# Kernel optimization log

Measured on AMD Instinct MI355X. Metric: run time of the kernel, lower is better.

The kernel has to match this reference:

```python
import jax, jax.numpy as jnp
import numpy as np

B, S, H = 2, 1024, 2048
D = 256          # index_dimension = min(index.embedding_dimension, hidden_size)
R = 32           # LoRA rank
K = 4            # index_k neighbors per query token
N_DB = 100000    # rows in the external index


def setup_inputs() -> dict:
    key = jax.random.key(0)
    ks = jax.random.split(key, 7)
    return {
        "hidden_states": jax.random.normal(ks[0], (B, S, H), jnp.float32),
        "db_keys": jax.random.normal(ks[1], (N_DB, D), jnp.float32),
        "db_values": jax.random.normal(ks[2], (N_DB, D), jnp.float32),
        "wq_in": jax.random.normal(ks[3], (H, R), jnp.float32) * 0.02,
        "wq_out": jax.random.normal(ks[4], (R, D), jnp.float32) * 0.02,
        "wv_in": jax.random.normal(ks[5], (D, R), jnp.float32) * 0.02,
        "wv_out": jax.random.normal(ks[6], (R, H), jnp.float32) * 0.02,
    }


def reference(hidden_states, db_keys, db_values, wq_in, wq_out, wv_in, wv_out):
    b, s, h = hidden_states.shape
    d = wq_out.shape[1]
    # query LoRA projection: hidden -> r -> index_dim
    q = (hidden_states @ wq_in) @ wq_out            # [B, S, D]

    # external k-NN lookup (exact L2 top-k over index table), no_grad in torch
    qf = q.reshape(b * s, d)                        # [B*S, D]
    qn = jnp.sum(qf * qf, axis=-1, keepdims=True)   # [B*S, 1]
    kn = jnp.sum(db_keys * db_keys, axis=-1)        # [N_DB]
    dist = qn - 2.0 * (qf @ db_keys.T) + kn[None, :]  # [B*S, N_DB]
    _, idx = jax.lax.top_k(-dist, K)                # [B*S, K] nearest neighbors

    # gather KV and reshape to [B, S*K, D] (matches torch view calls)
    kv_key = jax.lax.stop_gradient(db_keys[idx]).reshape(b, s * K, d)
    kv_val = jax.lax.stop_gradient(db_values[idx]).reshape(b, s * K, d)

    # SDPA, is_causal=True with Lq != Lk: top-left aligned tril mask (j <= i)
    scale = 1.0 / np.sqrt(d).astype(np.float32)
    scores = jnp.einsum('bqd,bkd->bqk', q, kv_key) * scale  # [B, S, S*K]
    mask = jnp.arange(s * K)[None, :] <= jnp.arange(s)[:, None]
    scores = jnp.where(mask[None, :, :], scores, jnp.finfo(scores.dtype).min)
    attn = jax.nn.softmax(scores, axis=-1)
    out = jnp.einsum('bqk,bkd->bqd', attn, kv_val)  # [B, S, D]

    # value LoRA projection: index_dim -> r -> hidden
    return (out @ wv_in) @ wv_out                   # [B, S, H]
```

## Files before the change

### kernel.cpp

```cpp
#include <hip/hip_runtime.h>
#include <cfloat>

#define B_   2
#define S_   1024
#define H_   2048
#define D_   256
#define R_   32
#define K_   4
#define NDB_ 100000

#define TSEL 256
#define NSEL (B_ * TSEL)

#define NCHUNK     112
#define CHUNK_ROWS 896
#define TILES      7
#define NT         128
#define MTM        32
#define QB_N       (NSEL / MTM)
#define MT         64
#define KC         64
#define LSTR       68

#define NEG_INF  (-3.0e38f)
#define IDX_MAX  0x7fffffff

#define TQ 4

#define OFF_Q     0
#define OFF_KN    0x200000
#define OFF_PS    0x280000
#define OFF_PI    0x360000
#define OFF_KVT   0x480000
#define OFF_KVV   0x680000
#define OFF_IDX   0x880000
#define OFF_DBK16 0xA00000

typedef unsigned short ushort_t;
typedef unsigned int   uint_t;
typedef __attribute__((ext_vector_type(8)))  __bf16 bf16x8;
typedef __attribute__((ext_vector_type(16))) float  f32x16;

__device__ __forceinline__ void ins4(float sc, int n, float s[4], int id[4]) {
  if (sc > s[3] || (sc == s[3] && n < id[3])) {
    s[3] = sc; id[3] = n;
#pragma unroll
    for (int k = 3; k > 0; --k) {
      if (s[k] > s[k - 1] || (s[k] == s[k - 1] && id[k] < id[k - 1])) {
        float ts = s[k]; s[k] = s[k - 1]; s[k - 1] = ts;
        int ti = id[k]; id[k] = id[k - 1]; id[k - 1] = ti;
      }
    }
  }
}

__device__ __forceinline__ uint_t bfpack(float a, float b) {
  uint_t ua = __float_as_uint(a), ub = __float_as_uint(b);
  ua = (ua + 0x7fffu + ((ua >> 16) & 1u)) >> 16;
  ub = (ub + 0x7fffu + ((ub >> 16) & 1u)) >> 16;
  return ua | (ub << 16);
}

__global__ __launch_bounds__(256) void k_prep(
    const float* __restrict__ hidden, const float* __restrict__ wq_in,
    const float* __restrict__ wq_out, float* __restrict__ q,
    const float* __restrict__ dbk, float* __restrict__ kn,
    ushort_t* __restrict__ dbk16T) {
  __shared__ __align__(16) char sm[32768];
  const int t = threadIdx.x;
  if (blockIdx.x < B_ * S_) {
    float* hrow = (float*)sm;
    float (*part)[R_] = (float(*)[R_])(sm + 8192);
    float* q1 = (float*)(sm + 9216);
    const int m = blockIdx.x;
    const float* hp = hidden + (size_t)m * H_;
    ((float4*)hrow)[t]       = ((const float4*)hp)[t];
    ((float4*)hrow)[t + 256] = ((const float4*)hp)[t + 256];
    __syncthreads();
    const int r = t & 31, c = t >> 5;
    float p = 0.f;
#pragma unroll 4
    for (int e = c * 256; e < c * 256 + 256; ++e)
      p = fmaf(hrow[e], wq_in[(size_t)e * R_ + r], p);
    part[c][r] = p;
    __syncthreads();
    if (t < R_) {
      float s = 0.f;
#pragma unroll
      for (int cc = 0; cc < 8; ++cc) s += part[cc][t];
      q1[t] = s;
    }
    __syncthreads();
    float acc = 0.f;
#pragma unroll
    for (int rr = 0; rr < R_; ++rr) acc = fmaf(q1[rr], wq_out[rr * D_ + t], acc);
    q[(size_t)m * D_ + t] = acc;
  } else {
    float* sT = (float*)sm;
    const int n32 = blockIdx.x - B_ * S_;
    {
      const int r = t >> 3, tc = t & 7;
      const float* rp = dbk + (size_t)(n32 * 32 + r) * D_;
      float s = 0.f;
#pragma unroll
      for (int k = 0; k < 8; ++k) {
        const int sl = tc + 8 * k;
        const float4 v = ((const float4*)rp)[sl];
        *(float4*)&sT[(r * 64 + (sl ^ (r & 7))) * 4] = v;
        s += v.x * v.x + v.y * v.y + v.z * v.z + v.w * v.w;
      }
      s += __shfl_down(s, 4, 8);
      s += __shfl_down(s, 2, 8);
      s += __shfl_down(s, 1, 8);
      if (tc == 0) kn[n32 * 32 + r] = s;
    }
    __syncthreads();
    {
      const int l = t & 63, w = t >> 6;
      const int row = l & 31, hc = l >> 5;
      uint4* dst = (uint4*)dbk16T + (size_t)n32 * 1024;
#pragma unroll
      for (int kk = 0; kk < 4; ++kk) {
        const int ks = kk * 4 + w;
        const int c = 2 * ks + hc;
        const int s0 = (2 * c) ^ (row & 7), s1 = (2 * c + 1) ^ (row & 7);
        const float4 a = *(const float4*)&sT[(row * 64 + s0) * 4];
        const float4 b = *(const float4*)&sT[(row * 64 + s1) * 4];
        uint4 pk;
        pk.x = bfpack(a.x, a.y); pk.y = bfpack(a.z, a.w);
        pk.z = bfpack(b.x, b.y); pk.w = bfpack(b.z, b.w);
        dst[(size_t)ks * 64 + l] = pk;
      }
    }
  }
}

__global__ __launch_bounds__(256) void k_compute_q(
    const float* __restrict__ hidden, const float* __restrict__ wq_in,
    const float* __restrict__ wq_out, float* __restrict__ q) {
  __shared__ float hrow[H_];
  __shared__ float part[8][R_];
  __shared__ float q1[R_];
  const int m = blockIdx.x;
  const int t = threadIdx.x;
  const float* hp = hidden + (size_t)m * H_;
  ((float4*)hrow)[t]       = ((const float4*)hp)[t];
  ((float4*)hrow)[t + 256] = ((const float4*)hp)[t + 256];
  __syncthreads();
  const int r = t & 31, c = t >> 5;
  float p = 0.f;
#pragma unroll 4
  for (int e = c * 256; e < c * 256 + 256; ++e)
    p = fmaf(hrow[e], wq_in[(size_t)e * R_ + r], p);
  part[c][r] = p;
  __syncthreads();
  if (t < R_) {
    float s = 0.f;
#pragma unroll
    for (int cc = 0; cc < 8; ++cc) s += part[cc][t];
    q1[t] = s;
  }
  __syncthreads();
  float acc = 0.f;
#pragma unroll
  for (int rr = 0; rr < R_; ++rr) acc = fmaf(q1[rr], wq_out[rr * D_ + t], acc);
  q[(size_t)m * D_ + t] = acc;
}

__global__ __launch_bounds__(256) void k_kn(const float* __restrict__ dbk,
                                            float* __restrict__ kn) {
  const int w = threadIdx.x >> 6, l = threadIdx.x & 63;
  const int n = blockIdx.x * 4 + w;
  if (n >= NDB_) return;
  const float4 v = ((const float4*)(dbk + (size_t)n * D_))[l];
  float s = v.x * v.x + v.y * v.y + v.z * v.z + v.w * v.w;
#pragma unroll
  for (int off = 32; off; off >>= 1) s += __shfl_down(s, off);
  if (l == 0) kn[n] = s;
}

__global__ __launch_bounds__(256, 7) void k_knn_mfma(
    const float* __restrict__ q, const ushort_t* __restrict__ dbk16T,
    const float* __restrict__ kn, float* __restrict__ pscore,
    int* __restrict__ pidx) {
  __shared__ __align__(16) char smem[16384 + CHUNK_ROWS * 4];
  ushort_t* sA  = (ushort_t*)smem;
  float*    knL = (float*)(smem + 16384);

  const int fid = blockIdx.x;
  const int xcd = fid & 7, idx8 = fid >> 3;
  const int chunk = xcd + 8 * (idx8 % 14);
  const int qb = idx8 / 14;

  const int tid = threadIdx.x;
  const int wv = tid >> 6, ln = tid & 63;
  const int lm = ln & 31, lh = ln >> 5;
  const int row_base = chunk * CHUNK_ROWS;

  {
    const int m = tid & 31, cg = tid >> 5;
    const int sq = qb * MTM + m;
    const float* qp = q + ((size_t)((sq >> 8) * S_ + (sq & 255))) * D_;
#pragma unroll
    for (int cc = 0; cc < 4; ++cc) {
      const int c = cg * 4 + cc;
      const float4 v0 = *(const float4*)(qp + c * 8);
      const float4 v1 = *(const float4*)(qp + c * 8 + 4);
      uint4 pk;
      pk.x = bfpack(v0.x, v0.y); pk.y = bfpack(v0.z, v0.w);
      pk.z = bfpack(v1.x, v1.y); pk.w = bfpack(v1.z, v1.w);
      *(uint4*)&sA[(m * 32 + (c ^ (m & 7))) * 8] = pk;
    }
  }
  for (int j = tid; j < CHUNK_ROWS; j += 256) {
    int rr = row_base + j; if (rr >= NDB_) rr = NDB_ - 1;
    knL[j] = kn[rr];
  }
  __syncthreads();

  float s40[4]; int i40[4];
#pragma unroll
  for (int k = 0; k < 4; ++k) { s40[k] = NEG_INF; i40[k] = IDX_MAX; }

  const int sw = lm & 7;
  const int abase0 = lm * 32;
  const int nbase = wv * 32 + 4 * lh;

  for (int tile = 0; tile < TILES; ++tile) {
    const int row0 = row_base + tile * NT;
    if (row0 >= NDB_) break;
    const int nw = row0 + wv * 32;
    if (nw >= NDB_) continue;

    f32x16 acc0;
#pragma unroll
    for (int r = 0; r < 16; ++r) acc0[r] = 0.f;

    const ushort_t* gw = dbk16T + (size_t)(nw >> 5) * 8192 + (size_t)ln * 8;
#pragma unroll
    for (int ks = 0; ks < 16; ++ks) {
      const bf16x8 bb = *(const bf16x8*)(gw + ks * 512);
      const int cs = (2 * ks + lh) ^ sw;
      const bf16x8 a0 = *(const bf16x8*)&sA[(abase0 + cs) * 8];
      acc0 = __builtin_amdgcn_mfma_f32_32x32x16_bf16(bb, a0, acc0, 0, 0, 0);
    }

#pragma unroll
    for (int g = 0; g < 4; ++g) {
      float v0[4]; int nn[4];
#pragma unroll
      for (int j = 0; j < 4; ++j) {
        const int r = g * 4 + j;
        const int off = (r & 3) + 8 * (r >> 2);
        const int nloc = nbase + off;
        const float knv = knL[tile * 128 + nloc];
        const int n = row0 + nloc;
        nn[j] = n;
        const float x0 = fmaf(2.f, acc0[r], -knv);
        v0[j] = (n < NDB_) ? x0 : NEG_INF;
      }
      const float m0 = fmaxf(fmaxf(v0[0], v0[1]), fmaxf(v0[2], v0[3]));
      if (m0 >= s40[3]) {
#pragma unroll
        for (int j = 0; j < 4; ++j) ins4(v0[j], nn[j], s40, i40);
      }
    }
  }

  __syncthreads();
  float* cs = (float*)smem;
  int*   ci = (int*)(smem + 4096);
  {
    const int st = wv * 2 + lh;
#pragma unroll
    for (int k = 0; k < 4; ++k) {
      cs[(lm * 8 + st) * 4 + k] = s40[k];
      ci[(lm * 8 + st) * 4 + k] = i40[k];
    }
  }
  __syncthreads();
  if (tid < MTM) {
    float fs[4]; int fi[4];
#pragma unroll
    for (int k = 0; k < 4; ++k) { fs[k] = NEG_INF; fi[k] = IDX_MAX; }
    for (int c = 0; c < 32; ++c)
      ins4(cs[tid * 32 + c], ci[tid * 32 + c], fs, fi);
    const int sq = qb * MTM + tid;
    float* po = pscore + ((size_t)sq * NCHUNK + chunk) * 4;
    int*   io = pidx   + ((size_t)sq * NCHUNK + chunk) * 4;
#pragma unroll
    for (int k = 0; k < 4; ++k) { po[k] = fs[k]; io[k] = fi[k]; }
  }
}

__global__ __launch_bounds__(256) void k_knn_partial(
    const float* __restrict__ q, const float* __restrict__ dbk,
    const float* __restrict__ kn, float* __restrict__ pscore,
    int* __restrict__ pidx) {
  __shared__ float smem[3 * KC * LSTR];
  float* sA  = smem;
  float* sB0 = smem + KC * LSTR;
  float* sB1 = smem + 2 * KC * LSTR;
  const int tid = threadIdx.x;
  const int tx = tid & 15, ty = tid >> 4;
  const int chunk = blockIdx.x, qb = blockIdx.y;
  const int arq = tid >> 2;
  const int aqd = (tid & 3) * 4;
  const int brk = tid >> 1;
  const int bh  = tid & 1;
  const int bcol = ((brk >> 3) << 2) | (brk & 3);
  float* sBw = (brk & 4) ? sB1 : sB0;
  const int sq_a = qb * MT + arq;
  const float* qsrc = q + ((size_t)((sq_a >> 8) * S_ + (sq_a & 255))) * D_;
  float s4[4][4]; int i4[4][4];
#pragma unroll
  for (int a = 0; a < 4; ++a)
#pragma unroll
    for (int b = 0; b < 4; ++b) { s4[a][b] = NEG_INF; i4[a][b] = IDX_MAX; }
  const int row_base = chunk * CHUNK_ROWS;
  for (int tile = 0; tile < TILES; ++tile) {
    const int row0 = row_base + tile * NT;
    if (row0 >= NDB_) break;
    int krow = row0 + brk; if (krow >= NDB_) krow = NDB_ - 1;
    const float* ksrc = dbk + (size_t)krow * D_;
    float acc[4][8];
#pragma unroll
    for (int a = 0; a < 4; ++a)
#pragma unroll
      for (int b = 0; b < 8; ++b) acc[a][b] = 0.f;
    for (int kc = 0; kc < 4; ++kc) {
      __syncthreads();
#pragma unroll
      for (int p = 0; p < 4; ++p) {
        const int kkl = p * 16 + aqd;
        const float4 v = *(const float4*)(qsrc + kc * KC + kkl);
        sA[(kkl + 0) * LSTR + arq] = v.x;
        sA[(kkl + 1) * LSTR + arq] = v.y;
        sA[(kkl + 2) * LSTR + arq] = v.z;
        sA[(kkl + 3) * LSTR + arq] = v.w;
      }
#pragma unroll
      for (int p = 0; p < 8; ++p) {
        const int kkl = bh * 32 + p * 4;
        const float4 v = *(const float4*)(ksrc + kc * KC + kkl);
        sBw[(kkl + 0) * LSTR + bcol] = v.x;
        sBw[(kkl + 1) * LSTR + bcol] = v.y;
        sBw[(kkl + 2) * LSTR + bcol] = v.z;
        sBw[(kkl + 3) * LSTR + bcol] = v.w;
      }
      __syncthreads();
#pragma unroll 4
      for (int kk = 0; kk < KC; ++kk) {
        const float4 a  = *(const float4*)&sA [kk * LSTR + ty * 4];
        const float4 b0 = *(const float4*)&sB0[kk * LSTR + tx * 4];
        const float4 b1 = *(const float4*)&sB1[kk * LSTR + tx * 4];
        const float av[4] = {a.x, a.y, a.z, a.w};
        const float bv[8] = {b0.x, b0.y, b0.z, b0.w, b1.x, b1.y, b1.z, b1.w};
#pragma unroll
        for (int qi = 0; qi < 4; ++qi)
#pragma unroll
          for (int nj = 0; nj < 8; ++nj)
            acc[qi][nj] = fmaf(av[qi], bv[nj], acc[qi][nj]);
      }
    }
#pragma unroll
    for (int nj = 0; nj < 8; ++nj) {
      const int n = row0 + tx * 8 + nj;
      if (n < NDB_) {
        const float knj = kn[n];
        ins4(2.f * acc[0][nj] - knj, n, s4[0], i4[0]);
        ins4(2.f * acc[1][nj] - knj, n, s4[1], i4[1]);
        ins4(2.f * acc[2][nj] - knj, n, s4[2], i4[2]);
        ins4(2.f * acc[3][nj] - knj, n, s4[3], i4[3]);
      }
    }
  }
  __syncthreads();
  float* cs = smem;
  int*   ci = (int*)(smem + 64 * 65);
#pragma unroll
  for (int qi = 0; qi < 4; ++qi)
#pragma unroll
    for (int k = 0; k < 4; ++k) {
      cs[(ty * 4 + qi) * 65 + tx * 4 + k] = s4[qi][k];
      ci[(ty * 4 + qi) * 65 + tx * 4 + k] = i4[qi][k];
    }
  __syncthreads();
  if (tid < 64) {
    float fs[4]; int fi[4];
#pragma unroll
    for (int k = 0; k < 4; ++k) { fs[k] = NEG_INF; fi[k] = IDX_MAX; }
    for (int c = 0; c < 64; ++c)
      ins4(cs[tid * 65 + c], ci[tid * 65 + c], fs, fi);
    const int sq = qb * MT + tid;
    float* po = pscore + ((size_t)sq * NCHUNK + chunk) * 4;
    int*   io = pidx   + ((size_t)sq * NCHUNK + chunk) * 4;
#pragma unroll
    for (int k = 0; k < 4; ++k) { po[k] = fs[k]; io[k] = fi[k]; }
  }
}

__global__ __launch_bounds__(64) void k_knn_merge4(const float* __restrict__ pscore,
                                                   const int* __restrict__ pidx,
                                                   int* __restrict__ knn_idx) {
  const int sq = blockIdx.x, l = threadIdx.x;
  float s4[4]; int i4[4];
#pragma unroll
  for (int k = 0; k < 4; ++k) { s4[k] = NEG_INF; i4[k] = IDX_MAX; }
  for (int c = l; c < NCHUNK * 4; c += 64)
    ins4(pscore[(size_t)sq * NCHUNK * 4 + c], pidx[(size_t)sq * NCHUNK * 4 + c], s4, i4);
#pragma unroll
  for (int r = 0; r < 4; ++r) {
    float s = s4[0]; int i = i4[0];
#pragma unroll
    for (int off = 32; off; off >>= 1) {
      float so = __shfl_down(s, off); int io = __shfl_down(i, off);
      if (so > s || (so == s && io < i)) { s = so; i = io; }
    }
    const float sw = __shfl(s, 0); const int iw = __shfl(i, 0);
    if (l == 0) knn_idx[sq * 4 + r] = iw;
    if (s4[0] == sw && i4[0] == iw) {
      s4[0] = s4[1]; i4[0] = i4[1];
      s4[1] = s4[2]; i4[1] = i4[2];
      s4[2] = s4[3]; i4[2] = i4[3];
      s4[3] = NEG_INF; i4[3] = IDX_MAX;
    }
  }
}

__global__ __launch_bounds__(256) void k_finalize(
    const float* __restrict__ pscore, const int* __restrict__ pidx,
    const float* __restrict__ q, const float* __restrict__ dbk,
    const float* __restrict__ dbv, const float* __restrict__ kn,
    float* __restrict__ kvT, float* __restrict__ kvV) {
  __shared__ int   cand16[16];
  __shared__ float scs[16];
  __shared__ int   sci[16];
  __shared__ int   top4[4];
  const int sq = blockIdx.x;
  const int t = threadIdx.x, wv = t >> 6, l = t & 63;

  if (wv == 0) {
    float s4[4]; int i4[4];
#pragma unroll
    for (int k = 0; k < 4; ++k) { s4[k] = NEG_INF; i4[k] = IDX_MAX; }
    for (int c = l; c < NCHUNK * 4; c += 64)
      ins4(pscore[(size_t)sq * NCHUNK * 4 + c],
           pidx[(size_t)sq * NCHUNK * 4 + c], s4, i4);
#pragma unroll
    for (int r = 0; r < 16; ++r) {
      float s = s4[0]; int i = i4[0];
#pragma unroll
      for (int off = 32; off; off >>= 1) {
        float so = __shfl_down(s, off); int io = __shfl_down(i, off);
        if (so > s || (so == s && io < i)) { s = so; i = io; }
      }
      const float sw = __shfl(s, 0); const int iw = __shfl(i, 0);
      if (l == 0) cand16[r] = iw;
      if (s4[0] == sw && i4[0] == iw) {
        s4[0] = s4[1]; i4[0] = i4[1];
        s4[1] = s4[2]; i4[1] = i4[2];
        s4[2] = s4[3]; i4[2] = i4[3];
        s4[3] = NEG_INF; i4[3] = IDX_MAX;
      }
    }
  }
  __syncthreads();

  const float* qp = q + ((size_t)((sq >> 8) * S_ + (sq & 255))) * D_;
  const float4 qv = ((const float4*)qp)[l];
  for (int cc = wv; cc < 16; cc += 4) {
    const int n = cand16[cc];
    const float4 kv = ((const float4*)(dbk + (size_t)n * D_))[l];
    float s = qv.x * kv.x + qv.y * kv.y + qv.z * kv.z + qv.w * kv.w;
#pragma unroll
    for (int off = 32; off; off >>= 1) s += __shfl_down(s, off);
    if (l == 0) { scs[cc] = 2.f * s - kn[n]; sci[cc] = n; }
  }
  __syncthreads();
  if (t == 0) {
    float s4[4]; int i4[4];
#pragma unroll
    for (int k = 0; k < 4; ++k) { s4[k] = NEG_INF; i4[k] = IDX_MAX; }
#pragma unroll
    for (int c = 0; c < 16; ++c) ins4(scs[c], sci[c], s4, i4);
#pragma unroll
    for (int k = 0; k < 4; ++k) top4[k] = i4[k];
  }
  __syncthreads();

  const int b = sq >> 8, tok = sq & 255;
  const int j = tok * 4 + wv;
  const int row = top4[wv];
  float* dstT = kvT + (size_t)b * D_ * 1024;
  const float4 kvk = ((const float4*)(dbk + (size_t)row * D_))[l];
  dstT[(4 * l + 0) * 1024 + j] = kvk.x;
  dstT[(4 * l + 1) * 1024 + j] = kvk.y;
  dstT[(4 * l + 2) * 1024 + j] = kvk.z;
  dstT[(4 * l + 3) * 1024 + j] = kvk.w;
  const float4 vv = ((const float4*)(dbv + (size_t)row * D_))[l];
  ((float4*)(kvV + ((size_t)b * 1024 + j) * D_))[l] = vv;
}

__global__ __launch_bounds__(256) void k_gather(const float* __restrict__ dbk,
                                                const float* __restrict__ dbv,
                                                const int* __restrict__ knn_idx,
                                                float* __restrict__ kvT,
                                                float* __restrict__ kvV) {
  const int b = blockIdx.x >> 6, j0 = (blockIdx.x & 63) * 16;
  const int w = threadIdx.x >> 6, l = threadIdx.x & 63;
  float* dstT = kvT + (size_t)b * D_ * 1024;
  float* dstV = kvV + (size_t)b * 1024 * D_;
  for (int jj = w; jj < 16; jj += 4) {
    const int j = j0 + jj;
    const int row = knn_idx[b * 1024 + j];
    const float4 kv = ((const float4*)(dbk + (size_t)row * D_))[l];
    dstT[(4 * l + 0) * 1024 + j] = kv.x;
    dstT[(4 * l + 1) * 1024 + j] = kv.y;
    dstT[(4 * l + 2) * 1024 + j] = kv.z;
    dstT[(4 * l + 3) * 1024 + j] = kv.w;
    const float4 vv = ((const float4*)(dbv + (size_t)row * D_))[l];
    ((float4*)(dstV + (size_t)j * D_))[l] = vv;
  }
}

template <int CMAX>
__device__ __forceinline__ void qk_dots(const float* __restrict__ kb, int t,
                                        const float (*qrow)[D_], float a[4][TQ]) {
#pragma unroll 2
  for (int d = 0; d < D_; d += 4) {
    float qv[TQ][4];
#pragma unroll
    for (int q = 0; q < TQ; ++q) {
      const float4 v = *(const float4*)&qrow[q][d];
      qv[q][0] = v.x; qv[q][1] = v.y; qv[q][2] = v.z; qv[q][3] = v.w;
    }
#pragma unroll
    for (int dd = 0; dd < 4; ++dd) {
      float kv[CMAX];
#pragma unroll
      for (int c = 0; c < CMAX; ++c)
        kv[c] = kb[(size_t)(d + dd) * 1024 + c * 256 + t];
#pragma unroll
      for (int c = 0; c < CMAX; ++c)
#pragma unroll
        for (int q = 0; q < TQ; ++q)
          a[c][q] = fmaf(qv[q][dd], kv[c], a[c][q]);
    }
  }
}

__global__ __launch_bounds__(256) void k_attn_out(
    const float* __restrict__ qarr, const float* __restrict__ kvT,
    const float* __restrict__ kvV, const float* __restrict__ wv_in,
    const float* __restrict__ wv_out, float* __restrict__ y) {
  __shared__ float qrow[TQ][D_];
  __shared__ float attw[TQ][1024];
  __shared__ float pvred[4][TQ][D_];
  __shared__ float redm[4][TQ], reds[4][TQ];
  __shared__ float t32s[TQ][R_];

  const int fid = blockIdx.x;
  const int b = fid & 1;
  const int g = fid >> 1;
  const int h = g >> 1;
  const int grp = (g & 1) ? (255 - h) : h;
  const int i0 = grp * TQ;
  const int t = threadIdx.x;
  const int w = t >> 6, l = t & 63;
  const int nkmax = i0 + TQ;
  const int cmax = (nkmax + 255) >> 8;

  {
    const float4 v = ((const float4*)(qarr + ((size_t)b * S_ + i0 + w) * D_))[l];
    float4 sv;
    sv.x = v.x * 0.0625f; sv.y = v.y * 0.0625f;
    sv.z = v.z * 0.0625f; sv.w = v.w * 0.0625f;
    ((float4*)&qrow[w][0])[l] = sv;
  }
  __syncthreads();

  const float* kb = kvT + (size_t)b * D_ * 1024;
  float a[4][TQ];
#pragma unroll
  for (int c = 0; c < 4; ++c)
#pragma unroll
    for (int q = 0; q < TQ; ++q) a[c][q] = 0.f;
  switch (cmax) {
    case 1: qk_dots<1>(kb, t, qrow, a); break;
    case 2: qk_dots<2>(kb, t, qrow, a); break;
    case 3: qk_dots<3>(kb, t, qrow, a); break;
    default: qk_dots<4>(kb, t, qrow, a); break;
  }
#pragma unroll
  for (int c = 0; c < 4; ++c)
    if (c < cmax)
#pragma unroll
      for (int q = 0; q < TQ; ++q)
        if (c * 256 + t > i0 + q) a[c][q] = NEG_INF;

#pragma unroll
  for (int q = 0; q < TQ; ++q) {
    float m = NEG_INF;
    for (int c = 0; c < cmax; ++c) m = fmaxf(m, a[c][q]);
#pragma unroll
    for (int off = 32; off; off >>= 1) m = fmaxf(m, __shfl_down(m, off));
    if (l == 0) redm[w][q] = m;
  }
  __syncthreads();
  float M[TQ];
#pragma unroll
  for (int q = 0; q < TQ; ++q)
    M[q] = fmaxf(fmaxf(redm[0][q], redm[1][q]), fmaxf(redm[2][q], redm[3][q]));
  float inv[TQ];
#pragma unroll
  for (int q = 0; q < TQ; ++q) {
    float s = 0.f;
    for (int c = 0; c < cmax; ++c) {
      const float p = (a[c][q] > 0.5f * NEG_INF) ? __expf(a[c][q] - M[q]) : 0.f;
      a[c][q] = p; s += p;
    }
#pragma unroll
    for (int off = 32; off; off >>= 1) s += __shfl_down(s, off);
    if (l == 0) reds[w][q] = s;
  }
  __syncthreads();
#pragma unroll
  for (int q = 0; q < TQ; ++q)
    inv[q] = 1.f / (reds[0][q] + reds[1][q] + reds[2][q] + reds[3][q]);
  for (int c = 0; c < cmax; ++c)
#pragma unroll
    for (int q = 0; q < TQ; ++q)
      attw[q][c * 256 + t] = a[c][q] * inv[q];
  __syncthreads();

  const float* vb = kvV + (size_t)b * 1024 * D_;
  float4 acc[TQ];
#pragma unroll
  for (int q = 0; q < TQ; ++q) acc[q] = make_float4(0.f, 0.f, 0.f, 0.f);
#pragma unroll 2
  for (int j = w; j < nkmax; j += 4) {
    const float4 v = ((const float4*)(vb + (size_t)j * D_))[l];
#pragma unroll
    for (int q = 0; q < TQ; ++q) {
      const float p = attw[q][j];
      acc[q].x = fmaf(p, v.x, acc[q].x);
      acc[q].y = fmaf(p, v.y, acc[q].y);
      acc[q].z = fmaf(p, v.z, acc[q].z);
      acc[q].w = fmaf(p, v.w, acc[q].w);
    }
  }
#pragma unroll
  for (int q = 0; q < TQ; ++q) ((float4*)&pvred[w][q][0])[l] = acc[q];
  __syncthreads();
  {
    const int qq = t >> 6;
    float4 s = make_float4(0.f, 0.f, 0.f, 0.f);
#pragma unroll
    for (int ww = 0; ww < 4; ++ww) {
      const float4 p = ((const float4*)&pvred[ww][qq][0])[l];
      s.x += p.x; s.y += p.y; s.z += p.z; s.w += p.w;
    }
    ((float4*)&qrow[qq][0])[l] = s;
  }
  __syncthreads();

  {
    const int qq = t >> 6, r = l & 31, hh = l >> 5;
    float p = 0.f;
    const float* ar = &qrow[qq][hh * 128];
    const float* wp = wv_in + (size_t)(hh * 128) * R_ + r;
#pragma unroll 8
    for (int d = 0; d < 128; ++d) p = fmaf(ar[d], wp[(size_t)d * R_], p);
    p += __shfl_down(p, 32);
    if (l < 32) t32s[qq][r] = p;
  }
  __syncthreads();

  const size_t ybase = ((size_t)b * S_ + i0) * H_;
  for (int ho = t; ho < H_; ho += 256) {
    float a0 = 0.f, a1 = 0.f, a2 = 0.f, a3 = 0.f;
#pragma unroll
    for (int rr = 0; rr < R_; ++rr) {
      const float wvv = wv_out[rr * H_ + ho];
      a0 = fmaf(t32s[0][rr], wvv, a0);
      a1 = fmaf(t32s[1][rr], wvv, a1);
      a2 = fmaf(t32s[2][rr], wvv, a2);
      a3 = fmaf(t32s[3][rr], wvv, a3);
    }
    y[ybase + ho]           = a0;
    y[ybase + H_ + ho]      = a1;
    y[ybase + 2 * H_ + ho]  = a2;
    y[ybase + 3 * H_ + ho]  = a3;
  }
}

extern "C" void kernel_launch(void* const* d_in, const int* in_sizes, int n_in,
                              void* d_out, int out_size, void* d_ws, size_t ws_size,
                              hipStream_t stream) {
  const float* hidden  = (const float*)d_in[0];
  const float* db_keys = (const float*)d_in[1];
  const float* db_vals = (const float*)d_in[2];
  const float* wq_in   = (const float*)d_in[3];
  const float* wq_out  = (const float*)d_in[4];
  const float* wv_in   = (const float*)d_in[5];
  const float* wv_out  = (const float*)d_in[6];
  float* out = (float*)d_out;

  char* ws = (char*)d_ws;
  float*    q      = (float*)(ws + OFF_Q);
  float*    kn     = (float*)(ws + OFF_KN);
  float*    ps     = (float*)(ws + OFF_PS);
  int*      pi     = (int*)  (ws + OFF_PI);
  int*      idx    = (int*)  (ws + OFF_IDX);
  float*    kvT    = (float*)(ws + OFF_KVT);
  float*    kvV    = (float*)(ws + OFF_KVV);
  ushort_t* dbk16  = (ushort_t*)(ws + OFF_DBK16);

  const size_t need = (size_t)OFF_DBK16 + (size_t)NDB_ * D_ * 2;

  if (ws_size >= need) {
    k_prep<<<B_ * S_ + NDB_ / 32, 256, 0, stream>>>(hidden, wq_in, wq_out, q,
                                                    db_keys, kn, dbk16);
    k_knn_mfma<<<NCHUNK * QB_N, 256, 0, stream>>>(q, dbk16, kn, ps, pi);
    k_finalize<<<NSEL, 256, 0, stream>>>(ps, pi, q, db_keys, db_vals, kn, kvT, kvV);
  } else {
    k_compute_q<<<B_ * S_, 256, 0, stream>>>(hidden, wq_in, wq_out, q);
    k_kn<<<(NDB_ + 3) / 4, 256, 0, stream>>>(db_keys, kn);
    k_knn_partial<<<dim3(NCHUNK, 8), 256, 0, stream>>>(q, db_keys, kn, ps, pi);
    k_knn_merge4<<<NSEL, 64, 0, stream>>>(ps, pi, idx);
    k_gather<<<2 * 64, 256, 0, stream>>>(db_keys, db_vals, idx, kvT, kvV);
  }
  k_attn_out<<<512, 256, 0, stream>>>(q, kvT, kvV, wv_in, wv_out, out);
}
```

Measured before the change: 470.2 us.

## Split causal attention over key chunks with flash-decoding style partial combine

Replaces the single attention kernel in the fast path with a split-K scheme. k_attn_part computes per-256-key-chunk partial softmax numerators, maxima and sums, skipping chunks that are fully masked. k_attn_comb rescales and merges the partials, then applies the value LoRA projection. This exposes more parallelism across chunks to balance the triangular causal workload, at the cost of writing and reading partial outputs through a workspace region that reuses the dbk16 buffer.

```diff
diff --git a/kernel.cpp b/kernel.cpp
--- a/kernel.cpp
+++ b/kernel.cpp
@@ -35,6 +35,9 @@
 #define OFF_KVV   0x680000
 #define OFF_IDX   0x880000
 #define OFF_DBK16 0xA00000
+#define OFF_PO   (OFF_DBK16)
+#define OFF_PM   (OFF_DBK16 + 0x2000000)
+#define OFF_PSUM (OFF_DBK16 + 0x2010000)
 
 typedef unsigned short ushort_t;
 typedef unsigned int   uint_t;
@@ -524,6 +527,177 @@
   }
 }
 
+__global__ __launch_bounds__(256) void k_attn_part(
+    const float* __restrict__ qarr, const float* __restrict__ kvT,
+    const float* __restrict__ kvV, float* __restrict__ po,
+    float* __restrict__ pm, float* __restrict__ ps) {
+  __shared__ float qrow[TQ][D_];
+  __shared__ float attw[TQ][256];
+  __shared__ float redm[4][TQ], reds[4][TQ];
+
+  const int fid = blockIdx.x;
+  const int b = fid & 1;
+  const int g = (fid >> 1) & 255;
+  const int c = fid >> 9;
+  const int i0 = g * TQ;
+  if (c * 256 >= i0 + TQ) return;
+  const int t = threadIdx.x;
+  const int w = t >> 6, l = t & 63;
+
+  {
+    const float4 v = ((const float4*)(qarr + ((size_t)b * S_ + i0 + w) * D_))[l];
+    float4 sv;
+    sv.x = v.x * 0.0625f; sv.y = v.y * 0.0625f;
+    sv.z = v.z * 0.0625f; sv.w = v.w * 0.0625f;
+    ((float4*)&qrow[w][0])[l] = sv;
+  }
+  __syncthreads();
+
+  const int j = c * 256 + t;
+  const float* kb = kvT + (size_t)b * D_ * 1024 + j;
+  float a[TQ];
+#pragma unroll
+  for (int q = 0; q < TQ; ++q) a[q] = 0.f;
+#pragma unroll 4
+  for (int d = 0; d < D_; d += 4) {
+    const float4 q0 = *(const float4*)&qrow[0][d];
+    const float4 q1 = *(const float4*)&qrow[1][d];
+    const float4 q2 = *(const float4*)&qrow[2][d];
+    const float4 q3 = *(const float4*)&qrow[3][d];
+    const float k0 = kb[(size_t)(d + 0) * 1024];
+    const float k1 = kb[(size_t)(d + 1) * 1024];
+    const float k2 = kb[(size_t)(d + 2) * 1024];
+    const float k3 = kb[(size_t)(d + 3) * 1024];
+    a[0] = fmaf(q0.w, k3, fmaf(q0.z, k2, fmaf(q0.y, k1, fmaf(q0.x, k0, a[0]))));
+    a[1] = fmaf(q1.w, k3, fmaf(q1.z, k2, fmaf(q1.y, k1, fmaf(q1.x, k0, a[1]))));
+    a[2] = fmaf(q2.w, k3, fmaf(q2.z, k2, fmaf(q2.y, k1, fmaf(q2.x, k0, a[2]))));
+    a[3] = fmaf(q3.w, k3, fmaf(q3.z, k2, fmaf(q3.y, k1, fmaf(q3.x, k0, a[3]))));
+  }
+#pragma unroll
+  for (int q = 0; q < TQ; ++q)
+    if (j > i0 + q) a[q] = NEG_INF;
+
+#pragma unroll
+  for (int q = 0; q < TQ; ++q) {
+    float mm = a[q];
+#pragma unroll
+    for (int off = 32; off; off >>= 1) mm = fmaxf(mm, __shfl_down(mm, off));
+    if (l == 0) redm[w][q] = mm;
+  }
+  __syncthreads();
+  float m[TQ];
+#pragma unroll
+  for (int q = 0; q < TQ; ++q)
+    m[q] = fmaxf(fmaxf(redm[0][q], redm[1][q]), fmaxf(redm[2][q], redm[3][q]));
+
+#pragma unroll
+  for (int q = 0; q < TQ; ++q) {
+    const float p = (a[q] > 0.5f * NEG_INF) ? __expf(a[q] - m[q]) : 0.f;
+    attw[q][t] = p;
+    float s = p;
+#pragma unroll
+    for (int off = 32; off; off >>= 1) s += __shfl_down(s, off);
+    if (l == 0) reds[w][q] = s;
+  }
+  __syncthreads();
+
+  const float* vb = kvV + ((size_t)b * 1024 + (size_t)c * 256) * D_;
+  float4 acc[TQ];
+#pragma unroll
+  for (int q = 0; q < TQ; ++q) acc[q] = make_float4(0.f, 0.f, 0.f, 0.f);
+#pragma unroll 2
+  for (int j2 = w; j2 < 256; j2 += 4) {
+    const float4 v = ((const float4*)(vb + (size_t)j2 * D_))[l];
+#pragma unroll
+    for (int q = 0; q < TQ; ++q) {
+      const float p = attw[q][j2];
+      acc[q].x = fmaf(p, v.x, acc[q].x);
+      acc[q].y = fmaf(p, v.y, acc[q].y);
+      acc[q].z = fmaf(p, v.z, acc[q].z);
+      acc[q].w = fmaf(p, v.w, acc[q].w);
+    }
+  }
+  float* pob = po + (size_t)fid * 4096 + w * 1024;
+#pragma unroll
+  for (int q = 0; q < TQ; ++q) ((float4*)(pob + q * 256))[l] = acc[q];
+  if (t == 0) {
+#pragma unroll
+    for (int q = 0; q < TQ; ++q) {
+      pm[fid * 4 + q] = m[q];
+      ps[fid * 4 + q] = reds[0][q] + reds[1][q] + reds[2][q] + reds[3][q];
+    }
+  }
+}
+
+__global__ __launch_bounds__(256) void k_attn_comb(
+    const float* __restrict__ po, const float* __restrict__ pm,
+    const float* __restrict__ ps, const float* __restrict__ wv_in,
+    const float* __restrict__ wv_out, float* __restrict__ y) {
+  __shared__ float aout[TQ][D_];
+  __shared__ float t32s[TQ][R_];
+  const int fid = blockIdx.x;
+  const int b = fid & 1, g = fid >> 1;
+  const int i0 = g * TQ;
+  const int cmax = (i0 + TQ + 255) >> 8;
+  const int t = threadIdx.x, w = t >> 6, l = t & 63;
+  const int q = w;
+
+  float M = NEG_INF;
+  for (int c = 0; c < cmax; ++c)
+    M = fmaxf(M, pm[((c << 9) | (g << 1) | b) * 4 + q]);
+  float S = 0.f;
+  float4 acc = make_float4(0.f, 0.f, 0.f, 0.f);
+  for (int c = 0; c < cmax; ++c) {
+    const int fa = (c << 9) | (g << 1) | b;
+    const float mc = pm[fa * 4 + q];
+    const float sc = (mc > 0.6f * NEG_INF) ? __expf(mc - M) : 0.f;
+    S += sc * ps[fa * 4 + q];
+    const float* pob = po + (size_t)fa * 4096 + q * 256;
+#pragma unroll
+    for (int w2 = 0; w2 < 4; ++w2) {
+      const float4 v = ((const float4*)(pob + w2 * 1024))[l];
+      acc.x = fmaf(sc, v.x, acc.x);
+      acc.y = fmaf(sc, v.y, acc.y);
+      acc.z = fmaf(sc, v.z, acc.z);
+      acc.w = fmaf(sc, v.w, acc.w);
+    }
+  }
+  const float inv = 1.f / S;
+  float4 r;
+  r.x = acc.x * inv; r.y = acc.y * inv; r.z = acc.z * inv; r.w = acc.w * inv;
+  ((float4*)&aout[q][0])[l] = r;
+  __syncthreads();
+
+  {
+    const int qq = t >> 6, rr = l & 31, hh = l >> 5;
+    float p = 0.f;
+    const float* ar = &aout[qq][hh * 128];
+    const float* wp = wv_in + (size_t)(hh * 128) * R_ + rr;
+#pragma unroll 8
+    for (int d = 0; d < 128; ++d) p = fmaf(ar[d], wp[(size_t)d * R_], p);
+    p += __shfl_down(p, 32);
+    if (l < 32) t32s[qq][rr] = p;
+  }
+  __syncthreads();
+
+  const size_t ybase = ((size_t)b * S_ + i0) * H_;
+  for (int ho = t; ho < H_; ho += 256) {
+    float a0 = 0.f, a1 = 0.f, a2 = 0.f, a3 = 0.f;
+#pragma unroll
+    for (int rr = 0; rr < R_; ++rr) {
+      const float wvv = wv_out[rr * H_ + ho];
+      a0 = fmaf(t32s[0][rr], wvv, a0);
+      a1 = fmaf(t32s[1][rr], wvv, a1);
+      a2 = fmaf(t32s[2][rr], wvv, a2);
+      a3 = fmaf(t32s[3][rr], wvv, a3);
+    }
+    y[ybase + ho]           = a0;
+    y[ybase + H_ + ho]      = a1;
+    y[ybase + 2 * H_ + ho]  = a2;
+    y[ybase + 3 * H_ + ho]  = a3;
+  }
+}
+
 template <int CMAX>
 __device__ __forceinline__ void qk_dots(const float* __restrict__ kb, int t,
                                         const float (*qrow)[D_], float a[4][TQ]) {
@@ -664,7 +838,6 @@
     ((float4*)&qrow[qq][0])[l] = s;
   }
   __syncthreads();
-
   {
     const int qq = t >> 6, r = l & 31, hh = l >> 5;
     float p = 0.f;
@@ -676,7 +849,6 @@
     if (l < 32) t32s[qq][r] = p;
   }
   __syncthreads();
-
   const size_t ybase = ((size_t)b * S_ + i0) * H_;
   for (int ho = t; ho < H_; ho += 256) {
     float a0 = 0.f, a1 = 0.f, a2 = 0.f, a3 = 0.f;
@@ -716,6 +888,9 @@
   float*    kvT    = (float*)(ws + OFF_KVT);
   float*    kvV    = (float*)(ws + OFF_KVV);
   ushort_t* dbk16  = (ushort_t*)(ws + OFF_DBK16);
+  float*    apo    = (float*)(ws + OFF_PO);
+  float*    apm    = (float*)(ws + OFF_PM);
+  float*    apsum  = (float*)(ws + OFF_PSUM);
 
   const size_t need = (size_t)OFF_DBK16 + (size_t)NDB_ * D_ * 2;
 
@@ -724,12 +899,14 @@
                                                     db_keys, kn, dbk16);
     k_knn_mfma<<<NCHUNK * QB_N, 256, 0, stream>>>(q, dbk16, kn, ps, pi);
     k_finalize<<<NSEL, 256, 0, stream>>>(ps, pi, q, db_keys, db_vals, kn, kvT, kvV);
+    k_attn_part<<<2048, 256, 0, stream>>>(q, kvT, kvV, apo, apm, apsum);
+    k_attn_comb<<<512, 256, 0, stream>>>(apo, apm, apsum, wv_in, wv_out, out);
   } else {
     k_compute_q<<<B_ * S_, 256, 0, stream>>>(hidden, wq_in, wq_out, q);
     k_kn<<<(NDB_ + 3) / 4, 256, 0, stream>>>(db_keys, kn);
     k_knn_partial<<<dim3(NCHUNK, 8), 256, 0, stream>>>(q, db_keys, kn, ps, pi);
     k_knn_merge4<<<NSEL, 64, 0, stream>>>(ps, pi, idx);
     k_gather<<<2 * 64, 256, 0, stream>>>(db_keys, db_vals, idx, kvT, kvV);
-  }
-  k_attn_out<<<512, 256, 0, stream>>>(q, kvT, kvV, wv_in, wv_out, out);
-}
+    k_attn_out<<<512, 256, 0, stream>>>(q, kvT, kvV, wv_in, wv_out, out);
+  }
+}
```

New measurement: 495.0 us. 1.05x slower.
